# Performance work log

Measured on AMD Instinct MI355X. Metric: run time of the kernel, lower is better.

Reference implementation:

```python
import jax, jax.numpy as jnp
import numpy as np

N, E = 20000, 320000
IN_C, HID, OUT_C, HEADS = 512, 32, 40, 8
NEG_SLOPE = 0.2


def setup_inputs() -> dict:
    key = jax.random.key(0)
    ks = jax.random.split(key, 10)
    x = jax.random.normal(ks[0], (N, IN_C), dtype=jnp.float32)
    edge_index = jax.random.randint(ks[1], (2, E), 0, N, dtype=jnp.int64)
    s1 = 1.0 / np.sqrt(IN_C)
    s2 = 1.0 / np.sqrt(HEADS * HID)
    return {
        "x": x,
        "edge_index": edge_index,
        "w1": jax.random.normal(ks[2], (IN_C, HEADS * HID), dtype=jnp.float32) * s1,
        "att_src1": jax.random.normal(ks[3], (HEADS, HID), dtype=jnp.float32) * s2,
        "att_dst1": jax.random.normal(ks[4], (HEADS, HID), dtype=jnp.float32) * s2,
        "b1": jnp.zeros((HEADS * HID,), dtype=jnp.float32),
        "w2": jax.random.normal(ks[5], (HEADS * HID, OUT_C), dtype=jnp.float32) * s2,
        "att_src2": jax.random.normal(ks[6], (1, OUT_C), dtype=jnp.float32) * 0.15,
        "att_dst2": jax.random.normal(ks[7], (1, OUT_C), dtype=jnp.float32) * 0.15,
        "b2": jnp.zeros((OUT_C,), dtype=jnp.float32),
    }


def gat_conv(x, src, dst, w, att_src, att_dst, bias, heads, out_c, concat):
    n = x.shape[0]
    h = (x @ w).reshape(n, heads, out_c)            # [N,H,C]
    a_s = jnp.sum(h * att_src, axis=-1)             # [N,H]
    a_d = jnp.sum(h * att_dst, axis=-1)             # [N,H]
    e = jax.nn.leaky_relu(a_s[src] + a_d[dst], NEG_SLOPE)  # [E,H]
    # segment softmax over destination nodes (self-loops guarantee nonempty)
    m = jax.ops.segment_max(e, dst, num_segments=n)
    e = jnp.exp(e - m[dst])
    z = jax.ops.segment_sum(e, dst, num_segments=n)
    alpha = e / (z[dst] + 1e-16)                    # [E,H]
    msg = alpha[:, :, None] * h[src]                # [E,H,C]
    out = jax.ops.segment_sum(msg, dst, num_segments=n)  # [N,H,C]
    out = out.reshape(n, heads * out_c) if concat else out.mean(axis=1)
    return out + bias


def reference(x, edge_index, w1, att_src1, att_dst1, b1, w2, att_src2, att_dst2, b2):
    n = x.shape[0]
    loops = jnp.arange(n, dtype=edge_index.dtype)
    src = jnp.concatenate([edge_index[0], loops])
    dst = jnp.concatenate([edge_index[1], loops])
    h = gat_conv(x, src, dst, w1, att_src1, att_dst1, b1, HEADS, HID, True)
    h = jax.nn.elu(h)
    out = gat_conv(h, src, dst, w2, att_src2, att_dst2, b2, 1, OUT_C, False)
    return jax.nn.log_softmax(out, axis=1)
```

## Files before the change

### kernel.cpp

```cpp
#include <hip/hip_runtime.h>
#include <hip/hip_bf16.h>
#include <math.h>

#define N_NODES 20000
#define N_EDGES 320000
#define ET (N_EDGES + N_NODES)
#define IN_C 512
#define HEADS 8
#define HID 32
#define HH (HEADS * HID)
#define OUT_C 40
#define NEG_SLOPE 0.2f

typedef __attribute__((ext_vector_type(8))) short short8;
typedef __attribute__((ext_vector_type(4))) float floatx4;

static __device__ __forceinline__ unsigned short f2bf(float f) {
  __hip_bfloat16 h = __float2bfloat16(f);
  return *(unsigned short*)&h;
}
static __device__ __forceinline__ float bf2f_lo(unsigned int u) {
  return __uint_as_float(u << 16);
}
static __device__ __forceinline__ float bf2f_hi(unsigned int u) {
  return __uint_as_float(u & 0xFFFF0000u);
}

#define WCONV_BLOCKS (IN_C * HH / 256)
#define COUNT_BLOCKS ((ET + 255) / 256)
__global__ __launch_bounds__(256) void prep_kernel(
    const float* __restrict__ w1, const int* __restrict__ ei,
    unsigned short* __restrict__ wbT, int* __restrict__ deg) {
  if (blockIdx.x < WCONV_BLOCKS) {
    int j = blockIdx.x * 256 + threadIdx.x;
    int k = j >> 8, n = j & 255;
    wbT[(size_t)n * IN_C + k] = f2bf(w1[j]);
  } else {
    int e = (blockIdx.x - WCONV_BLOCKS) * 256 + threadIdx.x;
    if (e < ET) {
      int dst = (e < N_EDGES) ? ei[N_EDGES + e] : (e - N_EDGES);
      atomicAdd(&deg[dst], 1);
    }
  }
}

#define BM 64
#define BN 128
#define BK 32
#define APAD 40
#define GY ((N_NODES + BM - 1) / BM)
#define GEMM_BLOCKS (2 * GY)
__global__ __launch_bounds__(256) void gemm1_kernel(
    const float* __restrict__ X, const unsigned short* __restrict__ BT,
    const float* __restrict__ bias, unsigned short* __restrict__ C,
    const int* __restrict__ deg, int* __restrict__ offs, int* __restrict__ cursor) {
  if (blockIdx.x >= GEMM_BLOCKS) {
    __shared__ int wsum[4];
    int t = threadIdx.x;
    int4 buf[20];
    int s = 0;
    if (t < 250) {
      const int4* dp = (const int4*)deg + t * 20;
#pragma unroll
      for (int i = 0; i < 20; i++) {
        buf[i] = dp[i];
        s += buf[i].x + buf[i].y + buf[i].z + buf[i].w;
      }
    }
    int lane = t & 63, w = t >> 6;
    int inc = s;
    for (int o = 1; o < 64; o <<= 1) {
      int u = __shfl_up(inc, o, 64);
      if (lane >= o) inc += u;
    }
    if (lane == 63) wsum[w] = inc;
    __syncthreads();
    int waveOff = 0;
    for (int i = 0; i < w; i++) waveOff += wsum[i];
    int running = waveOff + inc - s;
    if (t < 250) {
      int base = t * 80;
#pragma unroll
      for (int i = 0; i < 20; i++) {
        int4 v = buf[i];
        int4 o;
        o.x = running;
        o.y = o.x + v.x;
        o.z = o.y + v.y;
        o.w = o.z + v.z;
        running = o.w + v.w;
        *(int4*)(offs + base + i * 4) = o;
        *(int4*)(cursor + base + i * 4) = o;
      }
    }
    if (t == 0) offs[N_NODES] = ET;
    return;
  }
  __shared__ unsigned short As[BM][APAD];
  __shared__ unsigned short Bs[BN][APAD];
  const int tid = threadIdx.x;
  const int lane = tid & 63, wave = tid >> 6;
  const int wm = (wave & 1) * 32;
  const int wn = (wave >> 1) * 64;
  const int r16 = lane & 15, q = lane >> 4;
  const int bx = blockIdx.x & 1, by = blockIdx.x >> 1;
  const int rowBase = by * BM;
  const int colBase = bx * BN;
  floatx4 acc[2][4] = {};

  for (int k0 = 0; k0 < IN_C; k0 += BK) {
    {
      int row = tid >> 2, kc = (tid & 3) * 8;
      int arow = rowBase + row;
      float4 v0 = make_float4(0.f, 0.f, 0.f, 0.f), v1 = v0;
      if (arow < N_NODES) {
        const float* p = X + (size_t)arow * IN_C + k0 + kc;
        v0 = *(const float4*)p;
        v1 = *(const float4*)(p + 4);
      }
      unsigned short tmp[8] = {f2bf(v0.x), f2bf(v0.y), f2bf(v0.z), f2bf(v0.w),
                               f2bf(v1.x), f2bf(v1.y), f2bf(v1.z), f2bf(v1.w)};
      *(float4*)&As[row][kc] = *(const float4*)tmp;
    }
#pragma unroll
    for (int i = 0; i < 2; i++) {
      int c = tid + i * 256;
      int row = c >> 2, kc = (c & 3) * 8;
      float4 v = *(const float4*)(BT + (size_t)(colBase + row) * IN_C + k0 + kc);
      *(float4*)&Bs[row][kc] = v;
    }
    __syncthreads();
    short8 afrag[2], bfrag[4];
#pragma unroll
    for (int mt = 0; mt < 2; mt++)
      afrag[mt] = *(const short8*)&As[wm + mt * 16 + r16][q * 8];
#pragma unroll
    for (int nt = 0; nt < 4; nt++)
      bfrag[nt] = *(const short8*)&Bs[wn + nt * 16 + r16][q * 8];
#pragma unroll
    for (int mt = 0; mt < 2; mt++)
#pragma unroll
      for (int nt = 0; nt < 4; nt++)
        acc[mt][nt] = __builtin_amdgcn_mfma_f32_16x16x32_bf16(
            afrag[mt], bfrag[nt], acc[mt][nt], 0, 0, 0);
    __syncthreads();
  }
#pragma unroll
  for (int mt = 0; mt < 2; mt++) {
#pragma unroll
    for (int nt = 0; nt < 4; nt++) {
      int col = colBase + wn + nt * 16 + r16;
      float bb = bias[col];
#pragma unroll
      for (int r = 0; r < 4; r++) {
        int row = rowBase + wm + mt * 16 + q * 4 + r;
        if (row < N_NODES) C[(size_t)row * HH + col] = f2bf(acc[mt][nt][r] + bb);
      }
    }
  }
}

#define FILL_BLOCKS ((ET + 255) / 256)
#define ATTN1_BLOCKS (N_NODES / 4)
__global__ __launch_bounds__(256) void fill_attn1_kernel(
    const int* __restrict__ ei, int* __restrict__ cursor, int* __restrict__ csr,
    const unsigned short* __restrict__ h1b, const float* __restrict__ asrc,
    const float* __restrict__ adst, float* __restrict__ as1, float* __restrict__ ad1) {
  if (blockIdx.x < FILL_BLOCKS) {
    int e = blockIdx.x * 256 + threadIdx.x;
    if (e >= ET) return;
    int src, dst;
    if (e < N_EDGES) { src = ei[e]; dst = ei[N_EDGES + e]; }
    else { src = e - N_EDGES; dst = src; }
    int pos = atomicAdd(&cursor[dst], 1);
    csr[pos] = src;
  } else {
    int wave = threadIdx.x >> 6, lane = threadIdx.x & 63;
    int n = (blockIdx.x - FILL_BLOCKS) * 4 + wave;
    int c4 = lane * 4;
    uint2 raw = *(const uint2*)(h1b + (size_t)n * HH + c4);
    float h0 = bf2f_lo(raw.x), h1 = bf2f_hi(raw.x);
    float h2 = bf2f_lo(raw.y), h3 = bf2f_hi(raw.y);
    float4 sa = *(const float4*)(asrc + c4);
    float4 sd = *(const float4*)(adst + c4);
    float ps = h0 * sa.x + h1 * sa.y + h2 * sa.z + h3 * sa.w;
    float pd = h0 * sd.x + h1 * sd.y + h2 * sd.z + h3 * sd.w;
#pragma unroll
    for (int o = 4; o > 0; o >>= 1) {
      ps += __shfl_down(ps, o, 8);
      pd += __shfl_down(pd, o, 8);
    }
    if ((lane & 7) == 0) {
      as1[n * HEADS + (lane >> 3)] = ps;
      ad1[n * HEADS + (lane >> 3)] = pd;
    }
  }
}

__global__ __launch_bounds__(256) void agg1_kernel(
    const unsigned short* __restrict__ h1b, const float* __restrict__ as1,
    const float* __restrict__ ad1, const int* __restrict__ offs,
    const int* __restrict__ csr, const float* __restrict__ b1,
    float* __restrict__ h2) {
  int n = blockIdx.x * 4 + (threadIdx.x >> 6);
  int lane = threadIdx.x & 63;
  int half = lane >> 5;
  int sl = lane & 31;
  int c8 = sl * 8;
  int head = sl >> 2;
  int beg = offs[n], end = offs[n + 1];
  float ad = ad1[n * HEADS + head];
  float acc[8] = {};
  float l = 0.f;
#pragma unroll 2
  for (int k = beg + half; k < end; k += 2) {
    int src = csr[k];
    float e = as1[src * HEADS + head] + ad;
    e = (e > 0.f) ? e : NEG_SLOPE * e;
    float p = __expf(e);
    l += p;
    uint4 raw = *(const uint4*)(h1b + (size_t)src * HH + c8);
    acc[0] = fmaf(p, bf2f_lo(raw.x), acc[0]);
    acc[1] = fmaf(p, bf2f_hi(raw.x), acc[1]);
    acc[2] = fmaf(p, bf2f_lo(raw.y), acc[2]);
    acc[3] = fmaf(p, bf2f_hi(raw.y), acc[3]);
    acc[4] = fmaf(p, bf2f_lo(raw.z), acc[4]);
    acc[5] = fmaf(p, bf2f_hi(raw.z), acc[5]);
    acc[6] = fmaf(p, bf2f_lo(raw.w), acc[6]);
    acc[7] = fmaf(p, bf2f_hi(raw.w), acc[7]);
  }
#pragma unroll
  for (int j = 0; j < 8; j++) acc[j] += __shfl_xor(acc[j], 32, 64);
  l += __shfl_xor(l, 32, 64);
  if (half == 0) {
    float li = 1.f / (l + 1e-16f);
    float4 b0 = *(const float4*)(b1 + c8);
    float4 b4 = *(const float4*)(b1 + c8 + 4);
    float v[8];
    v[0] = acc[0] * li + b0.x; v[1] = acc[1] * li + b0.y;
    v[2] = acc[2] * li + b0.z; v[3] = acc[3] * li + b0.w;
    v[4] = acc[4] * li + b4.x; v[5] = acc[5] * li + b4.y;
    v[6] = acc[6] * li + b4.z; v[7] = acc[7] * li + b4.w;
#pragma unroll
    for (int j = 0; j < 8; j++) v[j] = (v[j] > 0.f) ? v[j] : expm1f(v[j]);
    *(float4*)(h2 + (size_t)n * HH + c8) = make_float4(v[0], v[1], v[2], v[3]);
    *(float4*)(h2 + (size_t)n * HH + c8 + 4) = make_float4(v[4], v[5], v[6], v[7]);
  }
}

__global__ __launch_bounds__(320) void gemm2_kernel(
    const float* __restrict__ h2, const float* __restrict__ w2,
    const float* __restrict__ b2, const float* __restrict__ asrc2,
    const float* __restrict__ adst2, float* __restrict__ h3,
    float* __restrict__ as2, float* __restrict__ ad2) {
  __shared__ float hs[32 * 257];
  __shared__ float ws2[HH * OUT_C];
  int t = threadIdx.x;
  int nodeBase = blockIdx.x * 32;
  const float* src = h2 + (size_t)nodeBase * HH;
  for (int idx = t; idx < 32 * 256; idx += 320) {
    int n = idx >> 8, k = idx & 255;
    hs[n * 257 + k] = src[idx];
  }
  for (int idx = t; idx < HH * OUT_C; idx += 320) ws2[idx] = w2[idx];
  __syncthreads();
  int c = t % OUT_C;
  int ng = t / OUT_C;
  float acc[4] = {0.f, 0.f, 0.f, 0.f};
  for (int k = 0; k < HH; k++) {
    float w = ws2[k * OUT_C + c];
#pragma unroll
    for (int i = 0; i < 4; i++) acc[i] += hs[(ng * 4 + i) * 257 + k] * w;
  }
  float bb = b2[c];
  float sa = asrc2[c], sd = adst2[c];
  float v[4];
#pragma unroll
  for (int i = 0; i < 4; i++) {
    v[i] = acc[i] + bb;
    h3[(size_t)(nodeBase + ng * 4 + i) * OUT_C + c] = v[i];
  }
  __syncthreads();
  float* sp = hs;
  float* sd2 = hs + OUT_C * 32;
#pragma unroll
  for (int i = 0; i < 4; i++) {
    sp[c * 32 + ng * 4 + i] = v[i] * sa;
    sd2[c * 32 + ng * 4 + i] = v[i] * sd;
  }
  __syncthreads();
  if (t < 32) {
    float ss = 0.f, dd = 0.f;
    for (int cc = 0; cc < OUT_C; cc++) {
      ss += sp[cc * 32 + t];
      dd += sd2[cc * 32 + t];
    }
    as2[nodeBase + t] = ss;
    ad2[nodeBase + t] = dd;
  }
}

__global__ __launch_bounds__(256) void agg2_kernel(
    const float* __restrict__ h3, const float* __restrict__ as2,
    const float* __restrict__ ad2, const int* __restrict__ offs,
    const int* __restrict__ csr, const float* __restrict__ b2,
    float* __restrict__ out) {
  int n = blockIdx.x * 4 + (threadIdx.x >> 6);
  int t = threadIdx.x & 63;
  bool act = (t < OUT_C);
  int beg = offs[n], end = offs[n + 1];
  float ad = ad2[n];
  float l = 0.f, acc = 0.f;
#pragma unroll 2
  for (int k = beg; k < end; k++) {
    int src = csr[k];
    float e = as2[src] + ad;
    e = (e > 0.f) ? e : NEG_SLOPE * e;
    float p = __expf(e);
    l += p;
    float hv = act ? h3[(size_t)src * OUT_C + t] : 0.f;
    acc = fmaf(p, hv, acc);
  }
  float v = acc / (l + 1e-16f) + (act ? b2[t] : 0.f);
  float x = act ? v : -INFINITY;
  float mx = x;
  for (int o = 32; o > 0; o >>= 1) mx = fmaxf(mx, __shfl_down(mx, o, 64));
  mx = __shfl(mx, 0, 64);
  float ex = act ? __expf(v - mx) : 0.f;
  float s = ex;
  for (int o = 32; o > 0; o >>= 1) s += __shfl_down(s, o, 64);
  s = __shfl(s, 0, 64);
  if (act) out[(size_t)n * OUT_C + t] = v - mx - logf(s);
}

extern "C" void kernel_launch(void* const* d_in, const int* in_sizes, int n_in,
                              void* d_out, int out_size, void* d_ws, size_t ws_size,
                              hipStream_t stream) {
  const float* x     = (const float*)d_in[0];
  const int*   ei    = (const int*)d_in[1];
  const float* w1    = (const float*)d_in[2];
  const float* asrc1 = (const float*)d_in[3];
  const float* adst1 = (const float*)d_in[4];
  const float* b1    = (const float*)d_in[5];
  const float* w2    = (const float*)d_in[6];
  const float* asrc2 = (const float*)d_in[7];
  const float* adst2 = (const float*)d_in[8];
  const float* b2    = (const float*)d_in[9];
  float* out = (float*)d_out;

  float* fw = (float*)d_ws;
  float* as1   = fw;  fw += (size_t)N_NODES * HEADS;
  float* ad1   = fw;  fw += (size_t)N_NODES * HEADS;
  float* h2    = fw;  fw += (size_t)N_NODES * HH;
  float* h3    = fw;  fw += (size_t)N_NODES * OUT_C;
  float* as2   = fw;  fw += N_NODES;
  float* ad2   = fw;  fw += N_NODES;
  unsigned short* h1b = (unsigned short*)fw;  fw += (size_t)N_NODES * HH / 2;
  unsigned short* wbT = (unsigned short*)fw;  fw += (size_t)IN_C * HH / 2;
  int* deg    = (int*)fw;
  int* offs   = deg + N_NODES;
  int* cursor = offs + N_NODES + 4;
  int* csr    = cursor + N_NODES;

  hipMemsetAsync(deg, 0, N_NODES * sizeof(int), stream);

  prep_kernel<<<WCONV_BLOCKS + COUNT_BLOCKS, 256, 0, stream>>>(w1, ei, wbT, deg);
  gemm1_kernel<<<GEMM_BLOCKS + 1, 256, 0, stream>>>(x, wbT, b1, h1b, deg, offs, cursor);
  fill_attn1_kernel<<<FILL_BLOCKS + ATTN1_BLOCKS, 256, 0, stream>>>(
      ei, cursor, csr, h1b, asrc1, adst1, as1, ad1);
  agg1_kernel<<<N_NODES / 4, 256, 0, stream>>>(h1b, as1, ad1, offs, csr, b1, h2);
  gemm2_kernel<<<N_NODES / 32, 320, 0, stream>>>(h2, w2, b2, asrc2, adst2, h3, as2, ad2);
  agg2_kernel<<<N_NODES / 4, 256, 0, stream>>>(h3, as2, ad2, offs, csr, b2, out);
}
```

Before: 242.7 us.

## Fuse layer-1 aggregation with layer-2 projection and attention logits

Merges the first GAT aggregation kernel with the second layer's small GEMM and attention-score computation. The ELU output row is kept in shared memory instead of being written to and reread from a global h2 buffer, and one kernel launch is removed. W2 is converted to a transposed bf16 copy in the prep kernel, and each block stages it in LDS (about 20KB) for the per-node 256x40 dot products. In exchange, the bf16 weights lower precision, and every one of the 5000 blocks redundantly reloads W2. The extra LDS per block may also reduce occupancy of the latency-bound gather loop.

```diff
diff --git a/kernel.cpp b/kernel.cpp
--- a/kernel.cpp
+++ b/kernel.cpp
@@ -27,16 +27,22 @@
 }
 
 #define WCONV_BLOCKS (IN_C * HH / 256)
+#define W2CONV_BLOCKS (HH * OUT_C / 256)
 #define COUNT_BLOCKS ((ET + 255) / 256)
 __global__ __launch_bounds__(256) void prep_kernel(
-    const float* __restrict__ w1, const int* __restrict__ ei,
-    unsigned short* __restrict__ wbT, int* __restrict__ deg) {
+    const float* __restrict__ w1, const float* __restrict__ w2,
+    const int* __restrict__ ei, unsigned short* __restrict__ wbT,
+    unsigned short* __restrict__ w2bT, int* __restrict__ deg) {
   if (blockIdx.x < WCONV_BLOCKS) {
     int j = blockIdx.x * 256 + threadIdx.x;
     int k = j >> 8, n = j & 255;
     wbT[(size_t)n * IN_C + k] = f2bf(w1[j]);
+  } else if (blockIdx.x < WCONV_BLOCKS + W2CONV_BLOCKS) {
+    int j = (blockIdx.x - WCONV_BLOCKS) * 256 + threadIdx.x;
+    int k = j / OUT_C, oc = j % OUT_C;
+    w2bT[oc * HH + k] = f2bf(w2[j]);
   } else {
-    int e = (blockIdx.x - WCONV_BLOCKS) * 256 + threadIdx.x;
+    int e = (blockIdx.x - WCONV_BLOCKS - W2CONV_BLOCKS) * 256 + threadIdx.x;
     if (e < ET) {
       int dst = (e < N_EDGES) ? ei[N_EDGES + e] : (e - N_EDGES);
       atomicAdd(&deg[dst], 1);
@@ -197,13 +203,27 @@
   }
 }
 
-__global__ __launch_bounds__(256) void agg1_kernel(
+#define W2ROW 260
+#define HROW 260
+__global__ __launch_bounds__(256) void layer1_fused_kernel(
     const unsigned short* __restrict__ h1b, const float* __restrict__ as1,
     const float* __restrict__ ad1, const int* __restrict__ offs,
     const int* __restrict__ csr, const float* __restrict__ b1,
-    float* __restrict__ h2) {
-  int n = blockIdx.x * 4 + (threadIdx.x >> 6);
-  int lane = threadIdx.x & 63;
+    const unsigned short* __restrict__ w2bT, const float* __restrict__ b2,
+    const float* __restrict__ asrc2, const float* __restrict__ adst2,
+    float* __restrict__ h3, float* __restrict__ as2, float* __restrict__ ad2) {
+  __shared__ unsigned short w2s[OUT_C * W2ROW];
+  __shared__ float hrow[4][HROW];
+  const int tid = threadIdx.x;
+#pragma unroll
+  for (int i = 0; i < 10; i++) {
+    int c = tid + i * 256;
+    int row = c >> 6, off = c & 63;
+    *(uint2*)&w2s[row * W2ROW + off * 4] = *(const uint2*)(w2bT + row * HH + off * 4);
+  }
+
+  int wave = tid >> 6, lane = tid & 63;
+  int n = blockIdx.x * 4 + wave;
   int half = lane >> 5;
   int sl = lane & 31;
   int c8 = sl * 8;
@@ -243,61 +263,32 @@
     v[6] = acc[6] * li + b4.z; v[7] = acc[7] * li + b4.w;
 #pragma unroll
     for (int j = 0; j < 8; j++) v[j] = (v[j] > 0.f) ? v[j] : expm1f(v[j]);
-    *(float4*)(h2 + (size_t)n * HH + c8) = make_float4(v[0], v[1], v[2], v[3]);
-    *(float4*)(h2 + (size_t)n * HH + c8 + 4) = make_float4(v[4], v[5], v[6], v[7]);
-  }
-}
-
-__global__ __launch_bounds__(320) void gemm2_kernel(
-    const float* __restrict__ h2, const float* __restrict__ w2,
-    const float* __restrict__ b2, const float* __restrict__ asrc2,
-    const float* __restrict__ adst2, float* __restrict__ h3,
-    float* __restrict__ as2, float* __restrict__ ad2) {
-  __shared__ float hs[32 * 257];
-  __shared__ float ws2[HH * OUT_C];
-  int t = threadIdx.x;
-  int nodeBase = blockIdx.x * 32;
-  const float* src = h2 + (size_t)nodeBase * HH;
-  for (int idx = t; idx < 32 * 256; idx += 320) {
-    int n = idx >> 8, k = idx & 255;
-    hs[n * 257 + k] = src[idx];
-  }
-  for (int idx = t; idx < HH * OUT_C; idx += 320) ws2[idx] = w2[idx];
+    *(float4*)&hrow[wave][c8] = make_float4(v[0], v[1], v[2], v[3]);
+    *(float4*)&hrow[wave][c8 + 4] = make_float4(v[4], v[5], v[6], v[7]);
+  }
   __syncthreads();
-  int c = t % OUT_C;
-  int ng = t / OUT_C;
-  float acc[4] = {0.f, 0.f, 0.f, 0.f};
-  for (int k = 0; k < HH; k++) {
-    float w = ws2[k * OUT_C + c];
-#pragma unroll
-    for (int i = 0; i < 4; i++) acc[i] += hs[(ng * 4 + i) * 257 + k] * w;
-  }
-  float bb = b2[c];
-  float sa = asrc2[c], sd = adst2[c];
-  float v[4];
-#pragma unroll
-  for (int i = 0; i < 4; i++) {
-    v[i] = acc[i] + bb;
-    h3[(size_t)(nodeBase + ng * 4 + i) * OUT_C + c] = v[i];
-  }
-  __syncthreads();
-  float* sp = hs;
-  float* sd2 = hs + OUT_C * 32;
-#pragma unroll
-  for (int i = 0; i < 4; i++) {
-    sp[c * 32 + ng * 4 + i] = v[i] * sa;
-    sd2[c * 32 + ng * 4 + i] = v[i] * sd;
-  }
-  __syncthreads();
-  if (t < 32) {
-    float ss = 0.f, dd = 0.f;
-    for (int cc = 0; cc < OUT_C; cc++) {
-      ss += sp[cc * 32 + t];
-      dd += sd2[cc * 32 + t];
-    }
-    as2[nodeBase + t] = ss;
-    ad2[nodeBase + t] = dd;
-  }
+
+  float val = 0.f, ps = 0.f, pd = 0.f;
+  if (lane < OUT_C) {
+    float hacc = 0.f;
+#pragma unroll 8
+    for (int g = 0; g < HH / 4; g++) {
+      float4 hv = *(const float4*)&hrow[wave][g * 4];
+      uint2 wv = *(const uint2*)&w2s[lane * W2ROW + g * 4];
+      hacc += hv.x * bf2f_lo(wv.x) + hv.y * bf2f_hi(wv.x)
+            + hv.z * bf2f_lo(wv.y) + hv.w * bf2f_hi(wv.y);
+    }
+    val = hacc + b2[lane];
+    h3[(size_t)n * OUT_C + lane] = val;
+    ps = val * asrc2[lane];
+    pd = val * adst2[lane];
+  }
+#pragma unroll
+  for (int o = 32; o > 0; o >>= 1) {
+    ps += __shfl_down(ps, o, 64);
+    pd += __shfl_down(pd, o, 64);
+  }
+  if (lane == 0) { as2[n] = ps; ad2[n] = pd; }
 }
 
 __global__ __launch_bounds__(256) void agg2_kernel(
@@ -351,12 +342,12 @@
   float* fw = (float*)d_ws;
   float* as1   = fw;  fw += (size_t)N_NODES * HEADS;
   float* ad1   = fw;  fw += (size_t)N_NODES * HEADS;
-  float* h2    = fw;  fw += (size_t)N_NODES * HH;
   float* h3    = fw;  fw += (size_t)N_NODES * OUT_C;
   float* as2   = fw;  fw += N_NODES;
   float* ad2   = fw;  fw += N_NODES;
-  unsigned short* h1b = (unsigned short*)fw;  fw += (size_t)N_NODES * HH / 2;
-  unsigned short* wbT = (unsigned short*)fw;  fw += (size_t)IN_C * HH / 2;
+  unsigned short* h1b  = (unsigned short*)fw;  fw += (size_t)N_NODES * HH / 2;
+  unsigned short* wbT  = (unsigned short*)fw;  fw += (size_t)IN_C * HH / 2;
+  unsigned short* w2bT = (unsigned short*)fw;  fw += (size_t)HH * OUT_C / 2;
   int* deg    = (int*)fw;
   int* offs   = deg + N_NODES;
   int* cursor = offs + N_NODES + 4;
@@ -364,11 +355,12 @@
 
   hipMemsetAsync(deg, 0, N_NODES * sizeof(int), stream);
 
-  prep_kernel<<<WCONV_BLOCKS + COUNT_BLOCKS, 256, 0, stream>>>(w1, ei, wbT, deg);
+  prep_kernel<<<WCONV_BLOCKS + W2CONV_BLOCKS + COUNT_BLOCKS, 256, 0, stream>>>(
+      w1, w2, ei, wbT, w2bT, deg);
   gemm1_kernel<<<GEMM_BLOCKS + 1, 256, 0, stream>>>(x, wbT, b1, h1b, deg, offs, cursor);
   fill_attn1_kernel<<<FILL_BLOCKS + ATTN1_BLOCKS, 256, 0, stream>>>(
       ei, cursor, csr, h1b, asrc1, adst1, as1, ad1);
-  agg1_kernel<<<N_NODES / 4, 256, 0, stream>>>(h1b, as1, ad1, offs, csr, b1, h2);
-  gemm2_kernel<<<N_NODES / 32, 320, 0, stream>>>(h2, w2, b2, asrc2, adst2, h3, as2, ad2);
+  layer1_fused_kernel<<<N_NODES / 4, 256, 0, stream>>>(
+      h1b, as1, ad1, offs, csr, b1, w2bT, b2, asrc2, adst2, h3, as2, ad2);
   agg2_kernel<<<N_NODES / 4, 256, 0, stream>>>(h3, as2, ad2, offs, csr, b2, out);
 }
```

Measured after the change: 232.8 us. -4.1%, faster.
